# Optimization experiments

Measured on AMD Instinct MI355X. Metric: run time of the kernel, lower is better.

## Reference

```python
import jax, jax.numpy as jnp
import numpy as np

D_MODEL = 1024
N_HEAD = 16


def setup_inputs() -> dict:
    key = jax.random.key(0)
    kx, kw = jax.random.split(key)
    x = jax.random.normal(kx, (4, 2048, D_MODEL), dtype=jnp.float32)
    # fused QKV projection weight, torch Linear: y = x @ W.T, W: [3*d_model, d_model]
    W_qkv = jax.random.normal(kw, (3 * D_MODEL, D_MODEL), dtype=jnp.float32) * (D_MODEL ** -0.5)
    return {"x": x, "W_qkv": W_qkv}


def reference(x, W_qkv):
    B, T, C = x.shape
    hd = C // N_HEAD
    qkv = jnp.einsum('btc,fc->btf', x, W_qkv)  # [B,T,3C]
    q, k, v = jnp.split(qkv, 3, axis=-1)
    # [B, H, T, hd]
    q = q.reshape(B, T, N_HEAD, hd).transpose(0, 2, 1, 3)
    k = k.reshape(B, T, N_HEAD, hd).transpose(0, 2, 1, 3)
    v = v.reshape(B, T, N_HEAD, hd).transpose(0, 2, 1, 3)
    scale = 1.0 / jnp.sqrt(jnp.asarray(hd, dtype=x.dtype))
    scores = jnp.einsum('bhqd,bhkd->bhqk', q, k) * scale  # [B,H,T,T]
    causal = jnp.tril(jnp.ones((T, T), dtype=bool))
    scores = jnp.where(causal, scores, jnp.asarray(-jnp.inf, dtype=scores.dtype))
    w = jax.nn.softmax(scores, axis=-1)
    out = jnp.einsum('bhqk,bhkd->bhqd', w, v)  # [B,H,T,hd]
    return out
```

## Files before the change

### kernel.cpp

```cpp
#include <hip/hip_runtime.h>
#include <hip/hip_bf16.h>
#include <math.h>

#define D_MODEL 1024
#define N_HEAD  16
#define HD      64
#define B_SZ    4
#define T_SEQ   2048
#define M_TOT   (B_SZ * T_SEQ)
#define N_TOT   (3 * D_MODEL)

typedef __bf16 bf16_t;
typedef __bf16 bf16x8 __attribute__((ext_vector_type(8)));
typedef __bf16 bf16x4 __attribute__((ext_vector_type(4)));
typedef __bf16 bf16x2 __attribute__((ext_vector_type(2)));
typedef float  f32x4  __attribute__((ext_vector_type(4)));
typedef float  f32x16 __attribute__((ext_vector_type(16)));
typedef int    i32x4  __attribute__((ext_vector_type(4)));

#define Q_PRESCALE 0.18033688011112042f

__global__ __launch_bounds__(256) void cvt_f32_bf16(const float* __restrict__ in,
                                                    bf16_t* __restrict__ out, int n4) {
  int i = blockIdx.x * blockDim.x + threadIdx.x;
  int stride = gridDim.x * blockDim.x;
  for (; i < n4; i += stride) {
    float4 v = ((const float4*)in)[i];
    bf16x4 o;
    o[0] = (bf16_t)v.x; o[1] = (bf16_t)v.y; o[2] = (bf16_t)v.z; o[3] = (bf16_t)v.w;
    ((bf16x4*)out)[i] = o;
  }
}

__global__ __launch_bounds__(256) void qkv_gemm(const bf16_t* __restrict__ xb,
                                                const bf16_t* __restrict__ wb,
                                                bf16_t* __restrict__ Q,
                                                bf16_t* __restrict__ Kf,
                                                bf16_t* __restrict__ Vf) {
  __shared__ alignas(16) bf16_t smem[24576];
  bf16_t* a_lds = smem;
  bf16_t* b_lds = smem + 12288;
  bf16_t* c_lds = smem;

  const int tid  = threadIdx.x;
  const int wave = tid >> 6;
  const int lane = tid & 63;
  const int bm = blockIdx.y * 128;
  const int bn = blockIdx.x * 128;
  const int sec = bn >> 10;

  f32x4 acc[4][4] = {};

  const int sRow  = lane >> 2;
  const int sCol8 = (lane & 3) ^ ((lane >> 3) & 3);
  const int fr = lane & 15;
  const int fk = lane >> 4;
  const int wm = (wave >> 1) * 64;
  const int wn = (wave & 1) * 64;

  auto stage = [&](int buf, int kk) {
#pragma unroll
    for (int c = 0; c < 2; ++c) {
      const int chunk = wave * 2 + c;
      const bf16_t* gA = &xb[(size_t)(bm + chunk * 16 + sRow) * D_MODEL + kk + sCol8 * 8];
      __builtin_amdgcn_global_load_lds(
          (__attribute__((address_space(1))) void*)(void*)gA,
          (__attribute__((address_space(3))) void*)&a_lds[buf * 4096 + chunk * 512], 16, 0, 0);
      const bf16_t* gB = &wb[(size_t)(bn + chunk * 16 + sRow) * D_MODEL + kk + sCol8 * 8];
      __builtin_amdgcn_global_load_lds(
          (__attribute__((address_space(1))) void*)(void*)gB,
          (__attribute__((address_space(3))) void*)&b_lds[buf * 4096 + chunk * 512], 16, 0, 0);
    }
  };

  auto loadFrags = [&](int buf, bf16x8 af[4], bf16x8 bfr[4]) {
#pragma unroll
    for (int mt = 0; mt < 4; ++mt) {
      const int row = wm + mt * 16 + fr;
      af[mt] = *(const bf16x8*)&a_lds[buf * 4096 + row * 32 + (fk ^ ((fr >> 1) & 3)) * 8];
    }
#pragma unroll
    for (int nt = 0; nt < 4; ++nt) {
      const int row = wn + nt * 16 + fr;
      bfr[nt] = *(const bf16x8*)&b_lds[buf * 4096 + row * 32 + (fk ^ ((fr >> 1) & 3)) * 8];
    }
  };

  auto mfmaAll = [&](bf16x8 af[4], bf16x8 bfr[4]) {
    __builtin_amdgcn_s_setprio(1);
#pragma unroll
    for (int mt = 0; mt < 4; ++mt)
#pragma unroll
      for (int nt = 0; nt < 4; ++nt)
        acc[mt][nt] = __builtin_amdgcn_mfma_f32_16x16x32_bf16(af[mt], bfr[nt], acc[mt][nt], 0, 0, 0);
    __builtin_amdgcn_s_setprio(0);
  };

  stage(0, 0);
  stage(1, 32);
  int cur = 0;
  for (int t = 0; t < 31; ++t) {
    asm volatile("s_waitcnt vmcnt(4)" ::: "memory");
    __builtin_amdgcn_s_barrier();
    __builtin_amdgcn_sched_barrier(0);
    bf16x8 af[4], bfr[4];
    loadFrags(cur, af, bfr);
    if (t < 30) stage((t + 2) % 3, (t + 2) * 32);
    mfmaAll(af, bfr);
    cur = (cur + 1) % 3;
  }
  asm volatile("s_waitcnt vmcnt(0)" ::: "memory");
  __builtin_amdgcn_s_barrier();
  __builtin_amdgcn_sched_barrier(0);
  {
    bf16x8 af[4], bfr[4];
    loadFrags(cur, af, bfr);
    mfmaAll(af, bfr);
  }

  const int cRowBase = (lane >> 4) * 4;
  const int cCol     = lane & 15;

  if (sec == 2) {
#pragma unroll
    for (int mt = 0; mt < 4; ++mt) {
#pragma unroll
      for (int nt = 0; nt < 4; ++nt) {
        const int hn = (bn & 1023) + wn + nt * 16 + cCol;
        const int h  = hn >> 6;
        const int d  = hn & 63;
        const int mbase = bm + wm + mt * 16 + cRowBase;
        const int b  = mbase >> 11;
        const int t0 = mbase & 2047;
        const int kvt = t0 >> 5, tt0 = t0 & 31;
        const int idx = (d >> 5) * 2 + (tt0 >> 4);
        const int h2  = (tt0 >> 3) & 1;
        const int j0  = tt0 & 7;
        bf16x4 pk;
        pk[0] = (bf16_t)acc[mt][nt][0]; pk[1] = (bf16_t)acc[mt][nt][1];
        pk[2] = (bf16_t)acc[mt][nt][2]; pk[3] = (bf16_t)acc[mt][nt][3];
        const size_t bhOff = (size_t)(b * N_HEAD + h) * (T_SEQ * HD);
        *(bf16x4*)&Vf[bhOff + (size_t)(((kvt * 4 + idx) * 64 + h2 * 32 + (d & 31)) * 8 + j0)] = pk;
      }
    }
  } else {
    __syncthreads();
    const float qs = (sec == 0) ? Q_PRESCALE : 1.0f;
#pragma unroll
    for (int mt = 0; mt < 4; ++mt)
#pragma unroll
      for (int nt = 0; nt < 4; ++nt)
#pragma unroll
        for (int r = 0; r < 4; ++r) {
          const int mloc = wm + mt * 16 + cRowBase + r;
          const int nloc = wn + nt * 16 + cCol;
          c_lds[mloc * 132 + nloc] = (bf16_t)(acc[mt][nt][r] * qs);
        }
    __syncthreads();

    const int row = tid >> 1;
    const int nh  = tid & 1;
    const int m = bm + row;
    const int b = m >> 11, t = m & 2047;
    const int h = ((bn & 1023) + nh * 64) >> 6;
    const size_t bhOff = (size_t)(b * N_HEAD + h) * (T_SEQ * HD);

    if (sec == 0) {
      bf16_t* qp = Q + bhOff + (size_t)t * HD;
#pragma unroll
      for (int o = 0; o < 16; ++o) {
        bf16x4 vv = *(const bf16x4*)&c_lds[row * 132 + nh * 64 + o * 4];
        *(bf16x4*)&qp[o * 4] = vv;
      }
    } else {
      const int kvt = t >> 5, lk = t & 31;
#pragma unroll
      for (int o = 0; o < 16; ++o) {
        const int d0 = o * 4;
        const int cc = d0 >> 4, h2 = (d0 >> 3) & 1, j0 = d0 & 7;
        bf16x4 vv = *(const bf16x4*)&c_lds[row * 132 + nh * 64 + d0];
        *(bf16x4*)&Kf[bhOff + (size_t)(((kvt * 4 + cc) * 64 + h2 * 32 + lk) * 8 + j0)] = vv;
      }
    }
  }
}

__device__ inline int pack_bf16(float lo, float hi) {
  bf16x2 v; v[0] = (bf16_t)lo; v[1] = (bf16_t)hi;
  return __builtin_bit_cast(int, v);
}
__device__ inline void permswap(int& a, int& b) {
  asm volatile("v_permlane32_swap_b32 %0, %1" : "+v"(a), "+v"(b));
}

__device__ inline void loadK4(bf16x8 k[4], const bf16_t* __restrict__ Kbase,
                              int kv0, int lane) {
  const bf16_t* p = Kbase + (size_t)(kv0 >> 5) * 2048 + lane * 8;
#pragma unroll
  for (int c = 0; c < 4; ++c) k[c] = *(const bf16x8*)(p + c * 512);
}
__device__ inline void loadV4(bf16x8 v[4], const bf16_t* __restrict__ Vbase,
                              int kv0, int lane) {
  const bf16_t* p = Vbase + (size_t)(kv0 >> 5) * 2048 + lane * 8;
#pragma unroll
  for (int idx = 0; idx < 4; ++idx) v[idx] = *(const bf16x8*)(p + idx * 512);
}

__global__ __launch_bounds__(256) void attn_fwd(const bf16_t* __restrict__ Q,
                                                const bf16_t* __restrict__ Kf,
                                                const bf16_t* __restrict__ Vf,
                                                float* __restrict__ out) {
  const int tid  = threadIdx.x;
  const int wave = tid >> 6;
  const int lane = tid & 63;
  const int l31  = lane & 31;
  const int hi   = lane >> 5;

  const int f    = blockIdx.x;
  const int bh   = ((f & 7) << 3) | ((f >> 3) & 7);
  const int bx   = f >> 6;
  const int c_lo = bx * 4 + wave;

  const bf16_t* Qp = Q  + (size_t)bh * T_SEQ * HD;
  const bf16_t* Kp = Kf + (size_t)bh * T_SEQ * HD;
  const bf16_t* Vp = Vf + (size_t)bh * T_SEQ * HD;
  float* op = out + (size_t)bh * T_SEQ * HD;

  for (int half = 0; half < 2; ++half) {
    const int chunk = half ? (63 - c_lo) : c_lo;
    const int q0 = chunk * 32;

    bf16x8 qf[4];
#pragma unroll
    for (int c = 0; c < 4; ++c)
      qf[c] = *(const bf16x8*)&Qp[(size_t)(q0 + l31) * HD + c * 16 + hi * 8];

    f32x16 o0 = {}, o1 = {};
    float m_run = -INFINITY;
    float l_run = 0.f;

    bf16x8 kA[4], vA[4];
    loadK4(kA, Kp, 0, lane);

    for (int kv0 = 0; kv0 <= q0; kv0 += 32) {
      loadV4(vA, Vp, kv0, lane);

      f32x16 st = {};
      __builtin_amdgcn_s_setprio(1);
#pragma unroll
      for (int c = 0; c < 4; ++c)
        st = __builtin_amdgcn_mfma_f32_32x32x16_bf16(kA[c], qf[c], st, 0, 0, 0);
      __builtin_amdgcn_s_setprio(0);

      const int nxt = (kv0 + 32 <= q0) ? kv0 + 32 : kv0;
      loadK4(kA, Kp, nxt, lane);

      if (kv0 == q0) {
#pragma unroll
        for (int r = 0; r < 16; ++r) {
          const int koff = (r & 3) + 8 * (r >> 2) + 4 * hi;
          st[r] = (koff > l31) ? -INFINITY : st[r];
        }
      }
      float pm = fmaxf(fmaxf(fmaxf(st[0], st[1]), fmaxf(st[2], st[3])),
                       fmaxf(fmaxf(st[4], st[5]), fmaxf(st[6], st[7])));
      pm = fmaxf(pm, fmaxf(fmaxf(fmaxf(st[8], st[9]), fmaxf(st[10], st[11])),
                           fmaxf(fmaxf(st[12], st[13]), fmaxf(st[14], st[15]))));

      if (__any(!(pm <= m_run + 8.f))) {
        const float pm_full = fmaxf(pm, __shfl_xor(pm, 32));
        const float m_new = fmaxf(m_run, pm_full);
        const float alpha = exp2f(m_run - m_new);
        m_run = m_new;
        l_run *= alpha;
#pragma unroll
        for (int r = 0; r < 16; ++r) {
          const int qr = (r & 3) + 8 * (r >> 2) + 4 * hi;
          const float av = __shfl(alpha, qr);
          o0[r] *= av; o1[r] *= av;
        }
      }

      float p[16];
#pragma unroll
      for (int r = 0; r < 16; ++r) p[r] = exp2f(st[r] - m_run);
      float s0 = (p[0] + p[1]) + (p[2] + p[3]);
      float s1 = (p[4] + p[5]) + (p[6] + p[7]);
      float s2 = (p[8] + p[9]) + (p[10] + p[11]);
      float s3 = (p[12] + p[13]) + (p[14] + p[15]);
      l_run += (s0 + s1) + (s2 + s3);

      int a01 = pack_bf16(p[0],  p[1]),  a23 = pack_bf16(p[2],  p[3]);
      int b01 = pack_bf16(p[4],  p[5]),  b23 = pack_bf16(p[6],  p[7]);
      int c01 = pack_bf16(p[8],  p[9]),  c23 = pack_bf16(p[10], p[11]);
      int d01 = pack_bf16(p[12], p[13]), d23 = pack_bf16(p[14], p[15]);
      permswap(a01, b01); permswap(a23, b23);
      permswap(c01, d01); permswap(c23, d23);
      i32x4 w1 = {a01, a23, b01, b23};
      i32x4 w2 = {c01, c23, d01, d23};
      bf16x8 f1 = __builtin_bit_cast(bf16x8, w1);
      bf16x8 f2 = __builtin_bit_cast(bf16x8, w2);

      __builtin_amdgcn_s_setprio(1);
      o0 = __builtin_amdgcn_mfma_f32_32x32x16_bf16(f1, vA[0], o0, 0, 0, 0);
      o0 = __builtin_amdgcn_mfma_f32_32x32x16_bf16(f2, vA[1], o0, 0, 0, 0);
      o1 = __builtin_amdgcn_mfma_f32_32x32x16_bf16(f1, vA[2], o1, 0, 0, 0);
      o1 = __builtin_amdgcn_mfma_f32_32x32x16_bf16(f2, vA[3], o1, 0, 0, 0);
      __builtin_amdgcn_s_setprio(0);
    }

    const float l_tot = l_run + __shfl_xor(l_run, 32);
    const float linv = 1.f / l_tot;
#pragma unroll
    for (int r = 0; r < 16; ++r) {
      const int qr = (r & 3) + 8 * (r >> 2) + 4 * hi;
      const float li = __shfl(linv, qr);
      op[(size_t)(q0 + qr) * HD + l31]      = o0[r] * li;
      op[(size_t)(q0 + qr) * HD + 32 + l31] = o1[r] * li;
    }
  }
}

extern "C" void kernel_launch(void* const* d_in, const int* in_sizes, int n_in,
                              void* d_out, int out_size, void* d_ws, size_t ws_size,
                              hipStream_t stream) {
  const float* x = (const float*)d_in[0];
  const float* W = (const float*)d_in[1];
  float* out = (float*)d_out;

  char* ws = (char*)d_ws;
  bf16_t* xb  = (bf16_t*)(ws);
  bf16_t* wb  = (bf16_t*)(ws + 16777216);
  bf16_t* Qb  = (bf16_t*)(ws + 16777216 + 6291456);
  bf16_t* Kfb = Qb + 8388608;
  bf16_t* Vfb = Kfb + 8388608;

  cvt_f32_bf16<<<2048, 256, 0, stream>>>(x, xb, (M_TOT * D_MODEL) / 4);
  cvt_f32_bf16<<<1024, 256, 0, stream>>>(W, wb, (N_TOT * D_MODEL) / 4);

  dim3 ggrid(N_TOT / 128, M_TOT / 128);
  qkv_gemm<<<ggrid, 256, 0, stream>>>(xb, wb, Qb, Kfb, Vfb);

  attn_fwd<<<512, 256, 0, stream>>>(Qb, Kfb, Vfb, out);
}
```

Baseline: 153.0 us.

## Split KV range across wave pairs and merge partial softmax via LDS

The attention kernel now assigns each 32-row query chunk to a pair of waves that each process half of the causal KV range, then merges their partial outputs, maxima and sums through shared memory using a flash-decoding-style combine. The grid grows from 512 to 2048 blocks with one chunk pair per block, and launch bounds request 4 blocks per CU. This aims to shorten the per-wave serial KV loop and improve load balance and occupancy. The cost is an extra LDS round trip, a block barrier, and half the waves sitting idle during the final write.

```diff
diff --git a/kernel.cpp b/kernel.cpp
--- a/kernel.cpp
+++ b/kernel.cpp
@@ -192,7 +192,6 @@
 __device__ inline void permswap(int& a, int& b) {
   asm volatile("v_permlane32_swap_b32 %0, %1" : "+v"(a), "+v"(b));
 }
-
 __device__ inline void loadK4(bf16x8 k[4], const bf16_t* __restrict__ Kbase,
                               int kv0, int lane) {
   const bf16_t* p = Kbase + (size_t)(kv0 >> 5) * 2048 + lane * 8;
@@ -206,43 +205,52 @@
   for (int idx = 0; idx < 4; ++idx) v[idx] = *(const bf16x8*)(p + idx * 512);
 }
 
-__global__ __launch_bounds__(256) void attn_fwd(const bf16_t* __restrict__ Q,
-                                                const bf16_t* __restrict__ Kf,
-                                                const bf16_t* __restrict__ Vf,
-                                                float* __restrict__ out) {
+__global__ __launch_bounds__(256, 4) void attn_fwd(const bf16_t* __restrict__ Q,
+                                                   const bf16_t* __restrict__ Kf,
+                                                   const bf16_t* __restrict__ Vf,
+                                                   float* __restrict__ out) {
+  __shared__ float o_sh[2][64][33];
+  __shared__ float m_sh[2][32];
+  __shared__ float l_sh[2][32];
+
   const int tid  = threadIdx.x;
   const int wave = tid >> 6;
   const int lane = tid & 63;
   const int l31  = lane & 31;
   const int hi   = lane >> 5;
 
-  const int f    = blockIdx.x;
-  const int bh   = ((f & 7) << 3) | ((f >> 3) & 7);
-  const int bx   = f >> 6;
-  const int c_lo = bx * 4 + wave;
+  const int f   = blockIdx.x;
+  const int bh  = ((f & 7) << 3) | ((f >> 3) & 7);
+  const int pr  = f >> 6;
+  const int grp = wave >> 1;
+  const int isWriter = wave & 1;
+  const int chunk = grp ? (63 - pr) : pr;
+  const int q0 = chunk * 32;
+  const int n  = chunk + 1;
+  const int h  = (n + 1) >> 1;
+  const int j0 = isWriter ? h : 0;
+  const int j1 = isWriter ? n : h;
 
   const bf16_t* Qp = Q  + (size_t)bh * T_SEQ * HD;
   const bf16_t* Kp = Kf + (size_t)bh * T_SEQ * HD;
   const bf16_t* Vp = Vf + (size_t)bh * T_SEQ * HD;
   float* op = out + (size_t)bh * T_SEQ * HD;
 
-  for (int half = 0; half < 2; ++half) {
-    const int chunk = half ? (63 - c_lo) : c_lo;
-    const int q0 = chunk * 32;
-
-    bf16x8 qf[4];
-#pragma unroll
-    for (int c = 0; c < 4; ++c)
-      qf[c] = *(const bf16x8*)&Qp[(size_t)(q0 + l31) * HD + c * 16 + hi * 8];
-
-    f32x16 o0 = {}, o1 = {};
-    float m_run = -INFINITY;
-    float l_run = 0.f;
-
+  bf16x8 qf[4];
+#pragma unroll
+  for (int c = 0; c < 4; ++c)
+    qf[c] = *(const bf16x8*)&Qp[(size_t)(q0 + l31) * HD + c * 16 + hi * 8];
+
+  f32x16 o0 = {}, o1 = {};
+  float m_run = -INFINITY;
+  float l_run = 0.f;
+
+  if (j0 < j1) {
     bf16x8 kA[4], vA[4];
-    loadK4(kA, Kp, 0, lane);
-
-    for (int kv0 = 0; kv0 <= q0; kv0 += 32) {
+    loadK4(kA, Kp, j0 * 32, lane);
+
+    for (int j = j0; j < j1; ++j) {
+      const int kv0 = j * 32;
       loadV4(vA, Vp, kv0, lane);
 
       f32x16 st = {};
@@ -252,7 +260,7 @@
         st = __builtin_amdgcn_mfma_f32_32x32x16_bf16(kA[c], qf[c], st, 0, 0, 0);
       __builtin_amdgcn_s_setprio(0);
 
-      const int nxt = (kv0 + 32 <= q0) ? kv0 + 32 : kv0;
+      const int nxt = (j + 1 < j1) ? (j + 1) * 32 : kv0;
       loadK4(kA, Kp, nxt, lane);
 
       if (kv0 == q0) {
@@ -308,15 +316,38 @@
       o1 = __builtin_amdgcn_mfma_f32_32x32x16_bf16(f2, vA[3], o1, 0, 0, 0);
       __builtin_amdgcn_s_setprio(0);
     }
-
-    const float l_tot = l_run + __shfl_xor(l_run, 32);
-    const float linv = 1.f / l_tot;
+  }
+
+  const float l_comb = l_run + __shfl_xor(l_run, 32);
+
+  if (isWriter) {
+#pragma unroll
+    for (int r = 0; r < 16; ++r) {
+      o_sh[grp][lane][r]      = o0[r];
+      o_sh[grp][lane][16 + r] = o1[r];
+    }
+    if (lane < 32) {
+      m_sh[grp][lane] = m_run;
+      l_sh[grp][lane] = l_comb;
+    }
+  }
+  __syncthreads();
+  if (!isWriter) {
 #pragma unroll
     for (int r = 0; r < 16; ++r) {
       const int qr = (r & 3) + 8 * (r >> 2) + 4 * hi;
-      const float li = __shfl(linv, qr);
-      op[(size_t)(q0 + qr) * HD + l31]      = o0[r] * li;
-      op[(size_t)(q0 + qr) * HD + 32 + l31] = o1[r] * li;
+      const float mB = m_sh[grp][qr];
+      const float lB = l_sh[grp][qr];
+      const float mA = __shfl(m_run, qr);
+      const float lA = __shfl(l_comb, qr);
+      const float mM = fmaxf(mA, mB);
+      const float aA = exp2f(mA - mM);
+      const float aB = exp2f(mB - mM);
+      const float li = 1.f / (lA * aA + lB * aB);
+      const float x0 = (o0[r] * aA + o_sh[grp][lane][r]      * aB) * li;
+      const float x1 = (o1[r] * aA + o_sh[grp][lane][16 + r] * aB) * li;
+      op[(size_t)(q0 + qr) * HD + l31]      = x0;
+      op[(size_t)(q0 + qr) * HD + 32 + l31] = x1;
     }
   }
 }
@@ -341,5 +372,5 @@
   dim3 ggrid(N_TOT / 128, M_TOT / 128);
   qkv_gemm<<<ggrid, 256, 0, stream>>>(xb, wb, Qb, Kfb, Vfb);
 
-  attn_fwd<<<512, 256, 0, stream>>>(Qb, Kfb, Vfb, out);
-}
+  attn_fwd<<<2048, 256, 0, stream>>>(Qb, Kfb, Vfb, out);
+}
```

Measured after the change: 151.3 us. No clear change (-1.1%).
